# Kernel tuning notes

Measured on AMD Instinct MI355X. Metric: run time of the kernel, lower is better.

The kernel has to match this reference:

```python
import jax, jax.numpy as jnp
import numpy as np

R_SPHERE = 3.0   # bounding_sphere_radius
NEAR = 0.0       # near_distance
FAR = 100.0      # far_distance
SECANT_STEPS = 4 # manifold_secant_steps
EPS = 1e-4
R0 = 1.0         # base radius of analytic manifold field


def setup_inputs() -> dict:
    key = jax.random.key(0)
    ks = jax.random.split(key, 6)
    B, R, L, H = 4, 8192, 4, 64
    rays_o = jax.random.normal(ks[0], (B, R, 3), dtype=jnp.float32) * 0.2  # origins inside sphere
    rd = jax.random.normal(ks[1], (B, R, 3), dtype=jnp.float32)
    rays_d = rd / jnp.linalg.norm(rd, axis=-1, keepdims=True)
    levels = jnp.linspace(0.5, -0.5, L, dtype=jnp.float32)  # manifold_levels parameter
    W1 = jax.random.normal(ks[2], (3, H), dtype=jnp.float32) * 0.3
    b1 = jnp.zeros((H,), dtype=jnp.float32)
    W2 = jax.random.normal(ks[3], (H, 1), dtype=jnp.float32) * 0.1
    b2 = jnp.zeros((1,), dtype=jnp.float32)
    rays_idx = jax.random.randint(ks[4], (B, R), 0, B, dtype=jnp.int64) if jax.config.jax_enable_x64 else jax.random.randint(ks[4], (B, R), 0, B, dtype=jnp.int32)
    mask_gt = jnp.ones((B, R), dtype=bool)
    return {"rays_o": rays_o, "rays_d": rays_d, "levels": levels, "W1": W1, "b1": b1,
            "W2": W2, "b2": b2, "mask_gt": mask_gt, "rays_idx": rays_idx, "num_samples": 64}


def _ray_march(rays_o, rays_d, levels, W1, b1, W2, b2, num_samples):
    B, Rn = rays_o.shape[:2]
    N = B * Rn
    L = levels.shape[0]
    o = rays_o.reshape(N, 3)
    d = rays_d.reshape(N, 3)

    def manifold_fn(x):
        # analytic stand-in for M(x_d, idx): scalar field + validity mask
        h = jnp.tanh(x @ W1 + b1)
        nrm = jnp.linalg.norm(x, axis=-1)
        s = (h @ W2)[..., 0] + b2[0] + (R0 - nrm)
        return s, nrm < R_SPHERE

    # ray-sphere intersection (unit-norm directions assumed, as in source)
    b = jnp.sum(o * d, axis=-1)
    c = jnp.sum(o * o, axis=-1) - R_SPHERE ** 2
    disc = b * b - c
    hit = disc > 0
    sq = jnp.sqrt(jnp.where(hit, disc, 1.0))
    d_near = jnp.maximum(-b - sq, NEAR)
    d_far = jnp.minimum(-b + sq, FAR)
    mask_bound = hit & (d_near < d_far)

    # stratified (uniform) depth samples, (N, S)
    t = jnp.linspace(0.0, 1.0, num_samples, dtype=rays_o.dtype)[None, :]
    ds = d_near[:, None] * (1 - t) + d_far[:, None] * t
    x_d = o[:, None, :] + d[:, None, :] * ds[..., None]  # (N, S, 3)
    scal, m_valid = manifold_fn(x_d)                      # (N, S)

    # --- find_closest_interval ---
    S = num_samples
    dep_f, dep_b = ds[:, :-1], ds[:, 1:]
    sc_f, sc_b = scal[:, :-1], scal[:, 1:]
    m_pair = m_valid[:, :-1] & m_valid[:, 1:]
    l3 = levels[None, :, None]                            # (1, L, 1)
    in_interval = (sc_f[:, None, :] >= l3) & (l3 >= sc_b[:, None, :]) & m_pair[:, None, :]
    rank = jnp.sign(l3 - sc_b[:, None, :]) * jnp.arange(S - 1, 0, -1, dtype=scal.dtype)
    ind_closest = jnp.argmax(rank, axis=2)                # (N, L)
    ind_lowest = jnp.broadcast_to(jnp.argmin(sc_b, axis=1)[:, None], (N, L))
    mask_surface = jnp.any(in_interval, axis=2)
    idx = jnp.where(mask_surface, ind_closest, ind_lowest)
    d_front = jnp.take_along_axis(dep_f, idx, axis=1)
    d_back = jnp.take_along_axis(dep_b, idx, axis=1)
    s_front = jnp.take_along_axis(sc_f, idx, axis=1)
    s_back = jnp.take_along_axis(sc_b, idx, axis=1)

    # --- find_exact_intersection ---
    lr = levels[None, :]                                  # (1, L)
    s_diff = s_front - s_back
    m_vdiff = jnp.abs(s_diff) > EPS
    mask_intersect = (s_front >= lr) & (lr >= s_back)
    mask_secant = mask_intersect & m_vdiff
    s_diff_safe = jnp.where(m_vdiff, s_diff, 1.0)
    d_secant = ((lr - s_back) * d_front + (s_front - lr) * d_back) / s_diff_safe
    d_init = jnp.where(mask_secant, d_secant, d_back)

    # secant refinement (fixed step count; masked full-array updates replace
    # torch's boolean-indexed subset updates with identical math on masked lanes)
    dfs, dbs, sfs, sbs, dcur = d_front, d_back, s_front, s_back, d_init
    for _ in range(SECANT_STEPS):
        x_mid = o[:, None, :] + dcur[..., None] * d[:, None, :]  # (N, L, 3)
        s_mid, mv = manifold_fn(x_mid)
        upf = (s_mid > lr) & mv
        upb = (s_mid < lr) & mv
        dfs = jnp.where(upf, dcur, dfs)
        sfs = jnp.where(upf, s_mid, sfs)
        dbs = jnp.where(upb, dcur, dbs)
        sbs = jnp.where(upb, s_mid, sbs)
        sd = sfs - sbs
        ok = jnp.abs(sd) > EPS
        dcur = jnp.where(ok, ((lr - sbs) * dfs + (sfs - lr) * dbs) / jnp.where(ok, sd, 1.0), dcur)
    d_intersect = jnp.where(mask_secant, dcur, d_init)

    # sort intersections by depth (use_presort=False branch)
    order = jnp.argsort(d_intersect, axis=1)
    d_intersect = jnp.take_along_axis(d_intersect, order, axis=1)
    mask_intersect = jnp.take_along_axis(mask_intersect, order, axis=1)

    dist = jnp.where(mask_bound[:, None], d_intersect, 0.0).reshape(B, Rn, L)
    mask = (mask_intersect & mask_bound[:, None]).reshape(B, Rn, L)
    return dist, mask


def reference(rays_o, rays_d, levels, W1, b1, W2, b2, mask_gt, rays_idx, num_samples):
    # mask_gt / rays_idx are unused in eval mode (use_gt_mask_when_training=False,
    # analytic manifold_fn ignores batch index), kept for signature fidelity.
    return _ray_march(rays_o, rays_d, levels, W1, b1, W2, b2, num_samples)
```

## Files before the change

kernel.cpp:

```cpp
#include <hip/hip_runtime.h>
#include <cstdint>

#define R_SPHEREf 3.0f
#define NEARf 0.0f
#define FARf 100.0f
#define SECANT_STEPS 4
#define EPSf 1e-4f
#define R0f 1.0f
#define Hh 64
#define Lc 4
#define Sn 64

#define C_HI 2.88539004325866699f
#define C_LO 3.8519227871e-08f

__global__ __launch_bounds__(256) void manifold_render_kernel(
    const float* __restrict__ rays_o, const float* __restrict__ rays_d,
    const float* __restrict__ levels, const float* __restrict__ W1,
    const float* __restrict__ b1, const float* __restrict__ W2,
    const float* __restrict__ b2, float* __restrict__ out, int N)
{
    __shared__ float4 abq[4][Hh];

    const int tid = threadIdx.x;
    const int wave = tid >> 6;
    const int lane = tid & 63;
    const int r = blockIdx.x * 4 + wave;
    if (r >= N) return;

    const float b2v = b2[0];
    float lvl[Lc];
#pragma unroll
    for (int j = 0; j < Lc; ++j) lvl[j] = levels[j];

    const float ox = rays_o[3 * r], oy = rays_o[3 * r + 1], oz = rays_o[3 * r + 2];
    const float dx = rays_d[3 * r], dy = rays_d[3 * r + 1], dz = rays_d[3 * r + 2];

    const float bq = ox * dx + oy * dy + oz * dz;
    const float cq = ox * ox + oy * oy + oz * oz - R_SPHEREf * R_SPHEREf;
    const float disc = bq * bq - cq;
    const bool hit = disc > 0.0f;
    const float sqv = __builtin_amdgcn_sqrtf(hit ? disc : 1.0f);
    const float d_near = fmaxf(-bq - sqv, NEARf);
    const float d_far  = fminf(-bq + sqv, FARf);
    const bool mask_bound = hit && (d_near < d_far);
    const float delta = (d_far - d_near) * (1.0f / 63.0f);

    const float w1x = W1[lane], w1y = W1[Hh + lane], w1z = W1[2 * Hh + lane];
    const float w2lane = W2[lane];
    const float Ah = __builtin_fmaf(oz, w1z, __builtin_fmaf(oy, w1y,
                     __builtin_fmaf(ox, w1x, b1[lane])));
    const float Bh = __builtin_fmaf(dz, w1z, __builtin_fmaf(dy, w1y, dx * w1x));
    const float A2 = __builtin_fmaf(Ah, C_LO, Ah * C_HI);
    const float B2 = __builtin_fmaf(Bh, C_LO, Bh * C_HI);
    const float zq = -2.0f * w2lane;
    const float zs = copysignf(fmaxf(fabsf(zq), 1e-30f), zq);
    const float rz = __builtin_amdgcn_rcpf(zs);
    const float Gh = __builtin_amdgcn_exp2f(B2 * (8.0f * delta));
    abq[wave][lane] = make_float4(A2, B2, rz, Gh);

    float w2sum = w2lane;
#pragma unroll
    for (int m = 1; m < 64; m <<= 1) w2sum += __shfl_xor(w2sum, m);
    const float sbase = w2sum + b2v + R0f;

    const int hg = lane >> 3;
    const int sl = lane & 7;
    const float dsl = __builtin_fmaf((float)sl, delta, d_near);

    const float4* __restrict__ ab = &abq[wave][0];
    float v[8], Gr[8], K[8];
#pragma unroll
    for (int j = 0; j < 8; ++j) {
        const float4 q = ab[hg + 8 * j];
        const float y = __builtin_fmaf(dsl, q.y, q.x);
        const float e0 = __builtin_amdgcn_exp2f(y);
        v[j]  = __builtin_fmaf(e0, q.z, q.z);
        Gr[j] = q.w;
        K[j]  = __builtin_fmaf(-q.z, q.w, q.z);
    }

    float mysum = 0.0f;
#pragma unroll
    for (int it = 0; it < 8; ++it) {
        if (it > 0) {
#pragma unroll
            for (int j = 0; j < 8; ++j) v[j] = __builtin_fmaf(v[j], Gr[j], K[j]);
        }
        const float n01 = v[0] + v[1], d01 = v[0] * v[1];
        const float n23 = v[2] + v[3], d23 = v[2] * v[3];
        const float numA = __builtin_fmaf(n23, d01, n01 * d23);
        const float denA = d01 * d23;
        const float n45 = v[4] + v[5], d45 = v[4] * v[5];
        const float n67 = v[6] + v[7], d67 = v[6] * v[7];
        const float numB = __builtin_fmaf(n67, d45, n45 * d67);
        const float denB = d45 * d67;
        float part = numA * __builtin_amdgcn_rcpf(denA);
        part = __builtin_fmaf(numB, __builtin_amdgcn_rcpf(denB), part);
        part += __shfl_xor(part, 8);
        part += __shfl_xor(part, 16);
        part += __shfl_xor(part, 32);
        if (it == hg) mysum = part;
    }

    const float t = (float)lane * (1.0f / 63.0f);
    const float dsv = d_near * (1.0f - t) + d_far * t;
    const float x0 = ox + dx * dsv, x1 = oy + dy * dsv, x2 = oz + dz * dsv;
    const float nrm = __builtin_amdgcn_sqrtf(x0 * x0 + x1 * x1 + x2 * x2);
    const float scal = (mysum + sbase) - nrm;
    const bool valid = nrm < R_SPHEREf;

    const float scb = __shfl_down(scal, 1);
    const int validn = __shfl_down((int)valid, 1);
    const bool is_int = lane < (Sn - 1);

    float keyv = is_int ? scb : INFINITY;
    int keyi = lane;
#pragma unroll
    for (int m = 1; m < 64; m <<= 1) {
        float ov = __shfl_xor(keyv, m);
        int oi = __shfl_xor(keyi, m);
        if (ov < keyv || (ov == keyv && oi < keyi)) { keyv = ov; keyi = oi; }
    }
    const int ind_lowest = keyi;

    const bool inint_base = is_int && valid && (validn != 0);

    bool mintb[Lc], msec[Lc];
    float dinit[Lc];
    float g_dfs = 0.f, g_dbs = 0.f, g_sfs = 0.f, g_sbs = 0.f, g_dcur = 0.f, g_lr = 0.f;
    const int gl = lane >> 4;

#pragma unroll
    for (int lv = 0; lv < Lc; ++lv) {
        const float l = lvl[lv];
        unsigned long long bP = __ballot(is_int && (scb < l));
        unsigned long long bZ = __ballot(is_int && (scb == l));
        unsigned long long bI = __ballot(inint_base && (scal >= l) && (l >= scb));
        int ind_closest = bP ? __builtin_ctzll(bP)
                             : (bZ ? __builtin_ctzll(bZ) : (Sn - 2));
        bool mask_surface = (bI != 0ULL);
        int idx = mask_surface ? ind_closest : ind_lowest;

        float d_front = __shfl(dsv, idx);
        float d_back  = __shfl(dsv, idx + 1);
        float s_front = __shfl(scal, idx);
        float s_back  = __shfl(scal, idx + 1);

        bool mi = (s_front >= l) && (l >= s_back);
        float sd = s_front - s_back;
        bool vd = fabsf(sd) > EPSf;
        bool ms = mi && vd;
        float num = (l - s_back) * d_front + (s_front - l) * d_back;
        float d_sec = num * __builtin_amdgcn_rcpf(vd ? sd : 1.0f);
        float di = ms ? d_sec : d_back;

        mintb[lv] = mi; msec[lv] = ms; dinit[lv] = di;
        if (gl == lv) {
            g_dfs = d_front; g_dbs = d_back; g_sfs = s_front; g_sbs = s_back;
            g_dcur = di; g_lr = l;
        }
    }

    const int sub = lane & 15;
    const float4 sq0 = ab[sub], sq1 = ab[sub + 16], sq2 = ab[sub + 32], sq3 = ab[sub + 48];

#pragma unroll
    for (int it = 0; it < SECANT_STEPS; ++it) {
        const float mx0 = ox + g_dcur * dx, mx1 = oy + g_dcur * dy, mx2 = oz + g_dcur * dz;
        const float mn = __builtin_amdgcn_sqrtf(mx0 * mx0 + mx1 * mx1 + mx2 * mx2);
        float part;
        {
            const float y0 = __builtin_fmaf(g_dcur, sq0.y, sq0.x);
            const float y1 = __builtin_fmaf(g_dcur, sq1.y, sq1.x);
            const float y2 = __builtin_fmaf(g_dcur, sq2.y, sq2.x);
            const float y3 = __builtin_fmaf(g_dcur, sq3.y, sq3.x);
            const float e0 = __builtin_amdgcn_exp2f(y0);
            const float e1 = __builtin_amdgcn_exp2f(y1);
            const float e2 = __builtin_amdgcn_exp2f(y2);
            const float e3 = __builtin_amdgcn_exp2f(y3);
            const float v0 = __builtin_fmaf(e0, sq0.z, sq0.z);
            const float v1 = __builtin_fmaf(e1, sq1.z, sq1.z);
            const float v2 = __builtin_fmaf(e2, sq2.z, sq2.z);
            const float v3 = __builtin_fmaf(e3, sq3.z, sq3.z);
            const float n01 = v0 + v1, d01 = v0 * v1;
            const float n23 = v2 + v3, d23 = v2 * v3;
            const float num = __builtin_fmaf(n23, d01, n01 * d23);
            const float den = d01 * d23;
            part = num * __builtin_amdgcn_rcpf(den);
        }
#pragma unroll
        for (int m = 1; m < 16; m <<= 1) part += __shfl_xor(part, m, 16);
        const float s_mid = (part + sbase) - mn;
        const bool mv = mn < R_SPHEREf;
        const bool upf = (s_mid > g_lr) && mv;
        const bool upb = (s_mid < g_lr) && mv;
        if (upf) { g_dfs = g_dcur; g_sfs = s_mid; }
        if (upb) { g_dbs = g_dcur; g_sbs = s_mid; }
        const float sd2 = g_sfs - g_sbs;
        const bool ok = fabsf(sd2) > EPSf;
        const float nd = (g_lr - g_sbs) * g_dfs + (g_sfs - g_lr) * g_dbs;
        if (ok) g_dcur = nd * __builtin_amdgcn_rcpf(sd2);
    }

    float v0g, v1g, v2g, v3g;
    {
        const float dc0 = __shfl(g_dcur, 0);
        const float dc1 = __shfl(g_dcur, 16);
        const float dc2 = __shfl(g_dcur, 32);
        const float dc3 = __shfl(g_dcur, 48);
        v0g = msec[0] ? dc0 : dinit[0];
        v1g = msec[1] ? dc1 : dinit[1];
        v2g = msec[2] ? dc2 : dinit[2];
        v3g = msec[3] ? dc3 : dinit[3];
    }
    int m0 = mintb[0], m1 = mintb[1], m2 = mintb[2], m3 = mintb[3];
    int i0 = 0, i1 = 1, i2 = 2, i3 = 3;

#define CSWAP(va, ia, ma, vb, ib, mb)                                    \
    { bool sw = (vb < va) || (vb == va && ib < ia);                      \
      if (sw) { float tv = va; va = vb; vb = tv;                         \
                int ti = ia; ia = ib; ib = ti;                           \
                int tm = ma; ma = mb; mb = tm; } }
    CSWAP(v0g, i0, m0, v1g, i1, m1);
    CSWAP(v2g, i2, m2, v3g, i3, m3);
    CSWAP(v0g, i0, m0, v2g, i2, m2);
    CSWAP(v1g, i1, m1, v3g, i3, m3);
    CSWAP(v1g, i1, m1, v2g, i2, m2);
#undef CSWAP

    const long long NL = (long long)N * Lc;
    if (lane < 2 * Lc) {
        const int k = lane & 3;
        const float dvs = (k == 0) ? v0g : (k == 1) ? v1g : (k == 2) ? v2g : v3g;
        const int   mms = (k == 0) ? m0 : (k == 1) ? m1 : (k == 2) ? m2 : m3;
        const bool isd = lane < Lc;
        const float val = isd ? (mask_bound ? dvs : 0.0f)
                              : ((mms && mask_bound) ? 1.0f : 0.0f);
        const long long off = (long long)r * Lc + k + (isd ? 0LL : NL);
        out[off] = val;
    }
}

extern "C" void kernel_launch(void* const* d_in, const int* in_sizes, int n_in,
                              void* d_out, int out_size, void* d_ws, size_t ws_size,
                              hipStream_t stream) {
    const float* rays_o = (const float*)d_in[0];
    const float* rays_d = (const float*)d_in[1];
    const float* levels = (const float*)d_in[2];
    const float* W1 = (const float*)d_in[3];
    const float* b1 = (const float*)d_in[4];
    const float* W2 = (const float*)d_in[5];
    const float* b2 = (const float*)d_in[6];
    float* out = (float*)d_out;

    const int N = in_sizes[0] / 3;
    const int blocks = (N + 3) / 4;
    manifold_render_kernel<<<blocks, 256, 0, stream>>>(
        rays_o, rays_d, levels, W1, b1, W2, b2, out, N);
}
```

Before: 110.7 us.

## Pack two rays per wavefront with half-wave split and ballot-based interval search

Each 64-lane wavefront now processes two rays, one per 32-lane half, with each lane holding two samples. Per-ray hidden-unit coefficients are computed for both rays and shared through LDS. The interval search switches from per-lane comparisons to bitmask operations assembled from ballots, and depths are recomputed analytically instead of shuffled. The secant refinement uses 8 lanes per level with 8 exps each, and divisions gain a Newton refinement step. This halves the number of wavefronts and the cross-lane reduction depth, at the cost of more registers per lane and extra ballot/shuffle logic.

```diff
diff --git a/kernel.cpp b/kernel.cpp
--- a/kernel.cpp
+++ b/kernel.cpp
@@ -14,27 +14,39 @@
 #define C_HI 2.88539004325866699f
 #define C_LO 3.8519227871e-08f
 
+typedef unsigned long long u64;
+
+__device__ __forceinline__ float fastdiv(float a, float b) {
+    float rcp = __builtin_amdgcn_rcpf(b);
+    rcp = __builtin_fmaf(rcp, __builtin_fmaf(-b, rcp, 1.0f), rcp);
+    return a * rcp;
+}
+
 __global__ __launch_bounds__(256) void manifold_render_kernel(
     const float* __restrict__ rays_o, const float* __restrict__ rays_d,
     const float* __restrict__ levels, const float* __restrict__ W1,
     const float* __restrict__ b1, const float* __restrict__ W2,
     const float* __restrict__ b2, float* __restrict__ out, int N)
 {
-    __shared__ float4 abq[4][Hh];
+    __shared__ float4 abq[4][2][Hh];
 
     const int tid = threadIdx.x;
     const int wave = tid >> 6;
     const int lane = tid & 63;
-    const int r = blockIdx.x * 4 + wave;
-    if (r >= N) return;
+    const int half = lane >> 5;
+    const int sl5  = lane & 31;
+    const int rbase = blockIdx.x * 8 + wave * 2;
+    if (rbase >= N) return;
+    const int r  = rbase + half;
+    const int rr = (r < N) ? r : (N - 1);
 
     const float b2v = b2[0];
     float lvl[Lc];
 #pragma unroll
     for (int j = 0; j < Lc; ++j) lvl[j] = levels[j];
 
-    const float ox = rays_o[3 * r], oy = rays_o[3 * r + 1], oz = rays_o[3 * r + 2];
-    const float dx = rays_d[3 * r], dy = rays_d[3 * r + 1], dz = rays_d[3 * r + 2];
+    const float ox = rays_o[3 * rr], oy = rays_o[3 * rr + 1], oz = rays_o[3 * rr + 2];
+    const float dx = rays_d[3 * rr], dy = rays_d[3 * rr + 1], dz = rays_d[3 * rr + 2];
 
     const float bq = ox * dx + oy * dy + oz * dz;
     const float cq = ox * ox + oy * oy + oz * oz - R_SPHEREf * R_SPHEREf;
@@ -48,112 +60,150 @@
 
     const float w1x = W1[lane], w1y = W1[Hh + lane], w1z = W1[2 * Hh + lane];
     const float w2lane = W2[lane];
-    const float Ah = __builtin_fmaf(oz, w1z, __builtin_fmaf(oy, w1y,
-                     __builtin_fmaf(ox, w1x, b1[lane])));
-    const float Bh = __builtin_fmaf(dz, w1z, __builtin_fmaf(dy, w1y, dx * w1x));
-    const float A2 = __builtin_fmaf(Ah, C_LO, Ah * C_HI);
-    const float B2 = __builtin_fmaf(Bh, C_LO, Bh * C_HI);
     const float zq = -2.0f * w2lane;
     const float zs = copysignf(fmaxf(fabsf(zq), 1e-30f), zq);
     const float rz = __builtin_amdgcn_rcpf(zs);
-    const float Gh = __builtin_amdgcn_exp2f(B2 * (8.0f * delta));
-    abq[wave][lane] = make_float4(A2, B2, rz, Gh);
+    {
+        const float Ah = __builtin_fmaf(oz, w1z, __builtin_fmaf(oy, w1y,
+                         __builtin_fmaf(ox, w1x, b1[lane])));
+        const float Bh = __builtin_fmaf(dz, w1z, __builtin_fmaf(dy, w1y, dx * w1x));
+        const float A2 = __builtin_fmaf(Ah, C_LO, Ah * C_HI);
+        const float B2 = __builtin_fmaf(Bh, C_LO, Bh * C_HI);
+        const float Gh = __builtin_amdgcn_exp2f(B2 * (8.0f * delta));
+        abq[wave][half][lane] = make_float4(A2, B2, rz, Gh);
+        const float oxo = __shfl_xor(ox, 32), oyo = __shfl_xor(oy, 32), ozo = __shfl_xor(oz, 32);
+        const float dxo = __shfl_xor(dx, 32), dyo = __shfl_xor(dy, 32), dzo = __shfl_xor(dz, 32);
+        const float dlo = __shfl_xor(delta, 32);
+        const float Aho = __builtin_fmaf(ozo, w1z, __builtin_fmaf(oyo, w1y,
+                          __builtin_fmaf(oxo, w1x, b1[lane])));
+        const float Bho = __builtin_fmaf(dzo, w1z, __builtin_fmaf(dyo, w1y, dxo * w1x));
+        const float A2o = __builtin_fmaf(Aho, C_LO, Aho * C_HI);
+        const float B2o = __builtin_fmaf(Bho, C_LO, Bho * C_HI);
+        const float Gho = __builtin_amdgcn_exp2f(B2o * (8.0f * dlo));
+        abq[wave][half ^ 1][lane] = make_float4(A2o, B2o, rz, Gho);
+    }
 
     float w2sum = w2lane;
 #pragma unroll
     for (int m = 1; m < 64; m <<= 1) w2sum += __shfl_xor(w2sum, m);
     const float sbase = w2sum + b2v + R0f;
 
-    const int hg = lane >> 3;
-    const int sl = lane & 7;
+    const int hg2 = (lane >> 3) & 3;
+    const int sl  = lane & 7;
     const float dsl = __builtin_fmaf((float)sl, delta, d_near);
 
-    const float4* __restrict__ ab = &abq[wave][0];
-    float v[8], Gr[8], K[8];
-#pragma unroll
-    for (int j = 0; j < 8; ++j) {
-        const float4 q = ab[hg + 8 * j];
+    const float4* __restrict__ ab = &abq[wave][half][0];
+    float v[16], G[16], K[16];
+#pragma unroll
+    for (int j = 0; j < 16; ++j) {
+        const float4 q = ab[hg2 + 4 * j];
         const float y = __builtin_fmaf(dsl, q.y, q.x);
         const float e0 = __builtin_amdgcn_exp2f(y);
-        v[j]  = __builtin_fmaf(e0, q.z, q.z);
-        Gr[j] = q.w;
-        K[j]  = __builtin_fmaf(-q.z, q.w, q.z);
-    }
-
-    float mysum = 0.0f;
+        v[j] = __builtin_fmaf(e0, q.z, q.z);
+        G[j] = q.w;
+        K[j] = __builtin_fmaf(-q.z, q.w, q.z);
+    }
+
+    float accA = 0.0f, accB = 0.0f;
 #pragma unroll
     for (int it = 0; it < 8; ++it) {
         if (it > 0) {
 #pragma unroll
-            for (int j = 0; j < 8; ++j) v[j] = __builtin_fmaf(v[j], Gr[j], K[j]);
-        }
-        const float n01 = v[0] + v[1], d01 = v[0] * v[1];
-        const float n23 = v[2] + v[3], d23 = v[2] * v[3];
-        const float numA = __builtin_fmaf(n23, d01, n01 * d23);
-        const float denA = d01 * d23;
-        const float n45 = v[4] + v[5], d45 = v[4] * v[5];
-        const float n67 = v[6] + v[7], d67 = v[6] * v[7];
-        const float numB = __builtin_fmaf(n67, d45, n45 * d67);
-        const float denB = d45 * d67;
-        float part = numA * __builtin_amdgcn_rcpf(denA);
-        part = __builtin_fmaf(numB, __builtin_amdgcn_rcpf(denB), part);
+            for (int j = 0; j < 16; ++j) v[j] = __builtin_fmaf(v[j], G[j], K[j]);
+        }
+        float part;
+        {
+            float tq[4];
+#pragma unroll
+            for (int qd = 0; qd < 4; ++qd) {
+                const float a = v[4 * qd], b = v[4 * qd + 1];
+                const float c = v[4 * qd + 2], d = v[4 * qd + 3];
+                const float n01 = a + b, d01 = a * b;
+                const float n23 = c + d, d23 = c * d;
+                const float num = __builtin_fmaf(n23, d01, n01 * d23);
+                const float den = d01 * d23;
+                tq[qd] = num * __builtin_amdgcn_rcpf(den);
+            }
+            part = (tq[0] + tq[1]) + (tq[2] + tq[3]);
+        }
         part += __shfl_xor(part, 8);
         part += __shfl_xor(part, 16);
-        part += __shfl_xor(part, 32);
-        if (it == hg) mysum = part;
-    }
-
-    const float t = (float)lane * (1.0f / 63.0f);
-    const float dsv = d_near * (1.0f - t) + d_far * t;
-    const float x0 = ox + dx * dsv, x1 = oy + dy * dsv, x2 = oz + dz * dsv;
-    const float nrm = __builtin_amdgcn_sqrtf(x0 * x0 + x1 * x1 + x2 * x2);
-    const float scal = (mysum + sbase) - nrm;
-    const bool valid = nrm < R_SPHEREf;
-
-    const float scb = __shfl_down(scal, 1);
-    const int validn = __shfl_down((int)valid, 1);
-    const bool is_int = lane < (Sn - 1);
-
-    float keyv = is_int ? scb : INFINITY;
-    int keyi = lane;
-#pragma unroll
-    for (int m = 1; m < 64; m <<= 1) {
-        float ov = __shfl_xor(keyv, m);
-        int oi = __shfl_xor(keyi, m);
-        if (ov < keyv || (ov == keyv && oi < keyi)) { keyv = ov; keyi = oi; }
-    }
-    const int ind_lowest = keyi;
-
-    const bool inint_base = is_int && valid && (validn != 0);
+        if (it == hg2)     accA = part;
+        if (it == hg2 + 4) accB = part;
+    }
+
+    const float tA = (float)sl5 * (1.0f / 63.0f);
+    const float dsvA = d_near * (1.0f - tA) + d_far * tA;
+    const float tB = (float)(sl5 + 32) * (1.0f / 63.0f);
+    const float dsvB = d_near * (1.0f - tB) + d_far * tB;
+    const float xA0 = ox + dx * dsvA, xA1 = oy + dy * dsvA, xA2 = oz + dz * dsvA;
+    const float xB0 = ox + dx * dsvB, xB1 = oy + dy * dsvB, xB2 = oz + dz * dsvB;
+    const float nrmA = __builtin_amdgcn_sqrtf(xA0 * xA0 + xA1 * xA1 + xA2 * xA2);
+    const float nrmB = __builtin_amdgcn_sqrtf(xB0 * xB0 + xB1 * xB1 + xB2 * xB2);
+    const float scalA = (accA + sbase) - nrmA;
+    const float scalB = (accB + sbase) - nrmB;
+    const bool validA = nrmA < R_SPHEREf;
+    const bool validB = nrmB < R_SPHEREf;
+
+    const u64 LO32 = 0xFFFFFFFFull;
+    const u64 mInt = 0x7FFFFFFFFFFFFFFFull;
+#define ASSEMBLE(bA, bB) (half ? (((bA) >> 32) | ((bB) & ~LO32)) \
+                               : (((bA) & LO32) | ((bB) << 32)))
+    const u64 bVA = __ballot(validA), bVB = __ballot(validB);
+    const u64 mV  = ASSEMBLE(bVA, bVB);
+    const u64 mIB = mV & (mV >> 1) & mInt;
+
+    float scbA = __shfl_down(scalA, 1);
+    const float sB0 = __shfl(scalB, half << 5);
+    if (sl5 == 31) scbA = sB0;
+    const float scbB = __shfl_down(scalB, 1);
+    const float keyA = scbA;
+    const float keyB = (sl5 < 31) ? scbB : INFINITY;
+    float mnv = fminf(keyA, keyB);
+#pragma unroll
+    for (int m = 1; m < 32; m <<= 1) mnv = fminf(mnv, __shfl_xor(mnv, m));
+    const u64 eqA = __ballot(keyA == mnv), eqB = __ballot(keyB == mnv);
+    const int ind_lowest = __builtin_ctzll(ASSEMBLE(eqA, eqB));
 
     bool mintb[Lc], msec[Lc];
     float dinit[Lc];
     float g_dfs = 0.f, g_dbs = 0.f, g_sfs = 0.f, g_sbs = 0.f, g_dcur = 0.f, g_lr = 0.f;
-    const int gl = lane >> 4;
+    const int gl = (lane >> 3) & 3;
 
 #pragma unroll
     for (int lv = 0; lv < Lc; ++lv) {
         const float l = lvl[lv];
-        unsigned long long bP = __ballot(is_int && (scb < l));
-        unsigned long long bZ = __ballot(is_int && (scb == l));
-        unsigned long long bI = __ballot(inint_base && (scal >= l) && (l >= scb));
-        int ind_closest = bP ? __builtin_ctzll(bP)
-                             : (bZ ? __builtin_ctzll(bZ) : (Sn - 2));
-        bool mask_surface = (bI != 0ULL);
-        int idx = mask_surface ? ind_closest : ind_lowest;
-
-        float d_front = __shfl(dsv, idx);
-        float d_back  = __shfl(dsv, idx + 1);
-        float s_front = __shfl(scal, idx);
-        float s_back  = __shfl(scal, idx + 1);
-
-        bool mi = (s_front >= l) && (l >= s_back);
-        float sd = s_front - s_back;
-        bool vd = fabsf(sd) > EPSf;
-        bool ms = mi && vd;
-        float num = (l - s_back) * d_front + (s_front - l) * d_back;
-        float d_sec = num * __builtin_amdgcn_rcpf(vd ? sd : 1.0f);
-        float di = ms ? d_sec : d_back;
+        const u64 bLA = __ballot(scalA < l),  bLB = __ballot(scalB < l);
+        const u64 bEA = __ballot(scalA == l), bEB = __ballot(scalB == l);
+        const u64 bL = ASSEMBLE(bLA, bLB);
+        const u64 bE = ASSEMBLE(bEA, bEB);
+        const u64 bP = (bL >> 1) & mInt;
+        const u64 bZ = (bE >> 1) & mInt;
+        const u64 bI = (~bL) & (bP | bZ) & mIB;
+        const int ind_closest = bP ? __builtin_ctzll(bP)
+                                   : (bZ ? __builtin_ctzll(bZ) : (Sn - 2));
+        const int idx  = bI ? ind_closest : ind_lowest;
+        const int idx1 = idx + 1;
+
+        const int src0 = (half << 5) | (idx & 31);
+        const float sfA = __shfl(scalA, src0), sfB = __shfl(scalB, src0);
+        const float s_front = (idx < 32) ? sfA : sfB;
+        const int src1 = (half << 5) | (idx1 & 31);
+        const float sbA2 = __shfl(scalA, src1), sbB2 = __shfl(scalB, src1);
+        const float s_back = (idx1 < 32) ? sbA2 : sbB2;
+
+        const float tf = (float)idx  * (1.0f / 63.0f);
+        const float d_front = d_near * (1.0f - tf) + d_far * tf;
+        const float tb = (float)idx1 * (1.0f / 63.0f);
+        const float d_back  = d_near * (1.0f - tb) + d_far * tb;
+
+        const bool mi = (s_front >= l) && (l >= s_back);
+        const float sd = s_front - s_back;
+        const bool vd = fabsf(sd) > EPSf;
+        const bool ms = mi && vd;
+        const float d_sec = fastdiv((l - s_back) * d_front + (s_front - l) * d_back,
+                                    vd ? sd : 1.0f);
+        const float di = ms ? d_sec : d_back;
 
         mintb[lv] = mi; msec[lv] = ms; dinit[lv] = di;
         if (gl == lv) {
@@ -162,35 +212,34 @@
         }
     }
 
-    const int sub = lane & 15;
-    const float4 sq0 = ab[sub], sq1 = ab[sub + 16], sq2 = ab[sub + 32], sq3 = ab[sub + 48];
+    const int sub = lane & 7;
+    const float4* __restrict__ ab2 = &abq[wave][half][0];
+    float4 sq[8];
+#pragma unroll
+    for (int j = 0; j < 8; ++j) sq[j] = ab2[sub + 8 * j];
 
 #pragma unroll
     for (int it = 0; it < SECANT_STEPS; ++it) {
         const float mx0 = ox + g_dcur * dx, mx1 = oy + g_dcur * dy, mx2 = oz + g_dcur * dz;
         const float mn = __builtin_amdgcn_sqrtf(mx0 * mx0 + mx1 * mx1 + mx2 * mx2);
-        float part;
-        {
-            const float y0 = __builtin_fmaf(g_dcur, sq0.y, sq0.x);
-            const float y1 = __builtin_fmaf(g_dcur, sq1.y, sq1.x);
-            const float y2 = __builtin_fmaf(g_dcur, sq2.y, sq2.x);
-            const float y3 = __builtin_fmaf(g_dcur, sq3.y, sq3.x);
-            const float e0 = __builtin_amdgcn_exp2f(y0);
-            const float e1 = __builtin_amdgcn_exp2f(y1);
-            const float e2 = __builtin_amdgcn_exp2f(y2);
-            const float e3 = __builtin_amdgcn_exp2f(y3);
-            const float v0 = __builtin_fmaf(e0, sq0.z, sq0.z);
-            const float v1 = __builtin_fmaf(e1, sq1.z, sq1.z);
-            const float v2 = __builtin_fmaf(e2, sq2.z, sq2.z);
-            const float v3 = __builtin_fmaf(e3, sq3.z, sq3.z);
-            const float n01 = v0 + v1, d01 = v0 * v1;
-            const float n23 = v2 + v3, d23 = v2 * v3;
-            const float num = __builtin_fmaf(n23, d01, n01 * d23);
-            const float den = d01 * d23;
-            part = num * __builtin_amdgcn_rcpf(den);
-        }
-#pragma unroll
-        for (int m = 1; m < 16; m <<= 1) part += __shfl_xor(part, m, 16);
+        float vv[8];
+#pragma unroll
+        for (int j = 0; j < 8; ++j) {
+            const float y = __builtin_fmaf(g_dcur, sq[j].y, sq[j].x);
+            const float e = __builtin_amdgcn_exp2f(y);
+            vv[j] = __builtin_fmaf(e, sq[j].z, sq[j].z);
+        }
+        float tp[4];
+#pragma unroll
+        for (int p = 0; p < 4; ++p) {
+            const float n = vv[2 * p] + vv[2 * p + 1];
+            const float d = vv[2 * p] * vv[2 * p + 1];
+            tp[p] = n * __builtin_amdgcn_rcpf(d);
+        }
+        float part = (tp[0] + tp[1]) + (tp[2] + tp[3]);
+        part += __shfl_xor(part, 1);
+        part += __shfl_xor(part, 2);
+        part += __shfl_xor(part, 4);
         const float s_mid = (part + sbase) - mn;
         const bool mv = mn < R_SPHEREf;
         const bool upf = (s_mid > g_lr) && mv;
@@ -199,16 +248,16 @@
         if (upb) { g_dbs = g_dcur; g_sbs = s_mid; }
         const float sd2 = g_sfs - g_sbs;
         const bool ok = fabsf(sd2) > EPSf;
-        const float nd = (g_lr - g_sbs) * g_dfs + (g_sfs - g_lr) * g_dbs;
-        if (ok) g_dcur = nd * __builtin_amdgcn_rcpf(sd2);
+        if (ok) g_dcur = fastdiv((g_lr - g_sbs) * g_dfs + (g_sfs - g_lr) * g_dbs, sd2);
     }
 
     float v0g, v1g, v2g, v3g;
     {
-        const float dc0 = __shfl(g_dcur, 0);
-        const float dc1 = __shfl(g_dcur, 16);
-        const float dc2 = __shfl(g_dcur, 32);
-        const float dc3 = __shfl(g_dcur, 48);
+        const int gb = half << 5;
+        const float dc0 = __shfl(g_dcur, gb);
+        const float dc1 = __shfl(g_dcur, gb + 8);
+        const float dc2 = __shfl(g_dcur, gb + 16);
+        const float dc3 = __shfl(g_dcur, gb + 24);
         v0g = msec[0] ? dc0 : dinit[0];
         v1g = msec[1] ? dc1 : dinit[1];
         v2g = msec[2] ? dc2 : dinit[2];
@@ -230,11 +279,11 @@
 #undef CSWAP
 
     const long long NL = (long long)N * Lc;
-    if (lane < 2 * Lc) {
-        const int k = lane & 3;
+    if (sl5 < 2 * Lc && r < N) {
+        const int k = sl5 & 3;
         const float dvs = (k == 0) ? v0g : (k == 1) ? v1g : (k == 2) ? v2g : v3g;
         const int   mms = (k == 0) ? m0 : (k == 1) ? m1 : (k == 2) ? m2 : m3;
-        const bool isd = lane < Lc;
+        const bool isd = sl5 < Lc;
         const float val = isd ? (mask_bound ? dvs : 0.0f)
                               : ((mms && mask_bound) ? 1.0f : 0.0f);
         const long long off = (long long)r * Lc + k + (isd ? 0LL : NL);
@@ -255,7 +304,7 @@
     float* out = (float*)d_out;
 
     const int N = in_sizes[0] / 3;
-    const int blocks = (N + 3) / 4;
+    const int blocks = (N + 7) / 8;
     manifold_render_kernel<<<blocks, 256, 0, stream>>>(
         rays_o, rays_d, levels, W1, b1, W2, b2, out, N);
 }
```

Measured after the change: 106.5 us, median of 2. 1.04x faster.
